# Optimization experiments

Measured on AMD Instinct MI355X. Metric: run time of the kernel, lower is better.

The kernel has to match this reference:

```python
import jax, jax.numpy as jnp
import numpy as np
from jax.ops import segment_sum

N_V = 50000   # vertices
N_E = 10000   # hyperedges
N_P = 800000  # incidence pairs
D_IN = 256
D_OUT = 256
NEG_SLOPE = 0.01


def setup_inputs() -> dict:
    key = jax.random.key(0)
    k1, k2, k3, k4, k5 = jax.random.split(key, 5)
    X = jax.random.normal(k1, (N_V, D_IN), dtype=jnp.float32)
    W = jax.random.normal(k2, (D_IN, D_OUT), dtype=jnp.float32) * (1.0 / np.sqrt(D_IN))
    b = jax.random.normal(k3, (D_OUT,), dtype=jnp.float32) * 0.01
    v_idx = jax.random.randint(k4, (N_P,), 0, N_V, dtype=jnp.int32)
    e_idx = jax.random.randint(k5, (N_P,), 0, N_E, dtype=jnp.int32)
    return {"X": X, "W": W, "b": b, "v_idx": v_idx, "e_idx": e_idx,
            "num_hyperedges": N_E}


def _mean_scatter(msg, idx, num_segments):
    # segment mean with count clamped to >=1 (empty segments -> 0)
    s = segment_sum(msg, idx, num_segments=num_segments)
    cnt = segment_sum(jnp.ones((msg.shape[0],), msg.dtype), idx,
                      num_segments=num_segments)
    return s / jnp.maximum(cnt, 1.0)[:, None]


def reference(X, W, b, v_idx, e_idx, num_hyperedges):
    # theta: linear projection  [N_V, D_OUT]
    H = X @ W + b
    # v2e mean: hyperedge features from member vertices
    e_feat = _mean_scatter(H[v_idx], e_idx, num_hyperedges)   # [N_E, D_OUT]
    # e2v mean: vertex features from incident hyperedges
    v_feat = _mean_scatter(e_feat[e_idx], v_idx, X.shape[0])  # [N_V, D_OUT]
    # leaky relu, default negative slope 0.01
    return jnp.where(v_feat >= 0, v_feat, NEG_SLOPE * v_feat)
```

## Files before the change

kernel.cpp:

```cpp
#include <hip/hip_runtime.h>

#define D 256
#define NEG_SLOPE 0.01f
#define E_PAD 192
#define V_PAD 64
#define EB 32
#define VB 64
#define NBE 313
#define NBV 782
#define CAP_E 3328
#define CAP_V 1536
#define CHUNK 8192
#define NS 8
#define DS 32

__device__ __forceinline__ unsigned short f2bf(float f) {
    union { float f; unsigned u; } x; x.f = f;
    unsigned r = x.u + 0x7fffu + ((x.u >> 16) & 1u);
    return (unsigned short)(r >> 16);
}
__device__ __forceinline__ float bf2f(unsigned short h) {
    union { float f; unsigned u; } x; x.u = ((unsigned)h) << 16;
    return x.f;
}

__global__ __launch_bounds__(256) void cvt_kernel(
        const float* __restrict__ X, unsigned short* __restrict__ Xhs, int n_v) {
    int i = blockIdx.x * blockDim.x + threadIdx.x;
    if (i >= n_v * 64) return;
    int v = i >> 6;
    int d4 = (i & 63) * 4;
    float4 val = *(const float4*)(X + (size_t)v * D + d4);
    ushort4 h;
    h.x = f2bf(val.x); h.y = f2bf(val.y); h.z = f2bf(val.z); h.w = f2bf(val.w);
    int s = d4 >> 5, wd = d4 & 31;
    *(ushort4*)(Xhs + (size_t)s * n_v * DS + (size_t)v * DS + wd) = h;
}

__global__ __launch_bounds__(256) void part_kernel(
        const int* __restrict__ v_idx, const int* __restrict__ e_idx,
        int* __restrict__ bc_e, int* __restrict__ bc_v,
        unsigned* __restrict__ pe, unsigned* __restrict__ pv, int n_p) {
    __shared__ int he[NBE], hv[NBV], beb[NBE], bvb[NBV];
    const int tid = threadIdx.x;
    const int base = blockIdx.x * CHUNK;
    for (int i = tid; i < NBE; i += 256) he[i] = 0;
    for (int i = tid; i < NBV; i += 256) hv[i] = 0;
    __syncthreads();
    #pragma unroll 4
    for (int r = 0; r < CHUNK / 256; ++r) {
        int p = base + r * 256 + tid;
        if (p < n_p) {
            atomicAdd(&he[e_idx[p] >> 5], 1);
            atomicAdd(&hv[v_idx[p] >> 6], 1);
        }
    }
    __syncthreads();
    for (int b = tid; b < NBE; b += 256) {
        int c = he[b];
        beb[b] = c ? atomicAdd(&bc_e[b], c) : 0;
        he[b] = 0;
    }
    for (int b = tid; b < NBV; b += 256) {
        int c = hv[b];
        bvb[b] = c ? atomicAdd(&bc_v[b], c) : 0;
        hv[b] = 0;
    }
    __syncthreads();
    #pragma unroll 4
    for (int r = 0; r < CHUNK / 256; ++r) {
        int p = base + r * 256 + tid;
        if (p < n_p) {
            int e = e_idx[p], v = v_idx[p];
            int b1 = e >> 5;
            int s1 = beb[b1] + atomicAdd(&he[b1], 1);
            if (s1 < CAP_E) pe[(size_t)b1 * CAP_E + s1] = (unsigned)v | ((unsigned)e << 16);
            int b2 = v >> 6;
            int s2 = bvb[b2] + atomicAdd(&hv[b2], 1);
            if (s2 < CAP_V) pv[(size_t)b2 * CAP_V + s2] = (unsigned)e | ((unsigned)v << 16);
        }
    }
}

__global__ __launch_bounds__(256) void build_e_kernel(
        const unsigned* __restrict__ pe, const int* __restrict__ bc_e,
        unsigned short* __restrict__ e_adj, int* __restrict__ e_fill, int n_e) {
    __shared__ unsigned short adj[EB * E_PAD];
    __shared__ int cnt[EB];
    const int b = blockIdx.x;
    const int tid = threadIdx.x;
    const int e0 = b * EB;
    int m = n_e - e0; if (m > EB) m = EB;
    for (int i = tid; i < EB; i += 256) cnt[i] = 0;
    __syncthreads();
    int total = bc_e[b]; if (total > CAP_E) total = CAP_E;
    for (int i = tid; i < total; i += 256) {
        unsigned p = pe[(size_t)b * CAP_E + i];
        int v = (int)(p & 0xFFFFu);
        int el = (int)(p >> 16) - e0;
        int s = atomicAdd(&cnt[el], 1);
        if (s < E_PAD) adj[el * E_PAD + s] = (unsigned short)v;
    }
    __syncthreads();
    unsigned* gout = (unsigned*)(e_adj + (size_t)e0 * E_PAD);
    const unsigned* lin = (const unsigned*)adj;
    int words = m * E_PAD / 2;
    for (int j = tid; j < words; j += 256) gout[j] = lin[j];
    for (int el = tid; el < m; el += 256) {
        int c = cnt[el]; if (c > E_PAD) c = E_PAD;
        e_fill[e0 + el] = c;
    }
}

__global__ __launch_bounds__(256) void v2e_kernel(
        const unsigned short* __restrict__ Xhs, const int* __restrict__ e_fill,
        const unsigned short* __restrict__ e_adj, float* __restrict__ Xagg,
        int n_e, int n_v) {
    const int s   = blockIdx.x;
    const int grp = threadIdx.x >> 4;
    const int sub = threadIdx.x & 15;
    const int e   = blockIdx.y * 16 + grp;
    if (e >= n_e) return;
    const unsigned short* tab = Xhs + (size_t)s * n_v * DS + (sub << 1);
    const unsigned short* adj = e_adj + (size_t)e * E_PAD;
    int cnt = e_fill[e];
    float ax = 0.f, ay = 0.f;
    int i = 0;
    for (; i + 8 <= cnt; i += 8) {
        int v0 = adj[i],   v1 = adj[i+1], v2 = adj[i+2], v3 = adj[i+3];
        int v4 = adj[i+4], v5 = adj[i+5], v6 = adj[i+6], v7 = adj[i+7];
        ushort2 a0 = *(const ushort2*)(tab + (size_t)v0 * DS);
        ushort2 a1 = *(const ushort2*)(tab + (size_t)v1 * DS);
        ushort2 a2 = *(const ushort2*)(tab + (size_t)v2 * DS);
        ushort2 a3 = *(const ushort2*)(tab + (size_t)v3 * DS);
        ushort2 a4 = *(const ushort2*)(tab + (size_t)v4 * DS);
        ushort2 a5 = *(const ushort2*)(tab + (size_t)v5 * DS);
        ushort2 a6 = *(const ushort2*)(tab + (size_t)v6 * DS);
        ushort2 a7 = *(const ushort2*)(tab + (size_t)v7 * DS);
        ax += (bf2f(a0.x) + bf2f(a1.x)) + (bf2f(a2.x) + bf2f(a3.x))
            + (bf2f(a4.x) + bf2f(a5.x)) + (bf2f(a6.x) + bf2f(a7.x));
        ay += (bf2f(a0.y) + bf2f(a1.y)) + (bf2f(a2.y) + bf2f(a3.y))
            + (bf2f(a4.y) + bf2f(a5.y)) + (bf2f(a6.y) + bf2f(a7.y));
    }
    for (; i < cnt; ++i) {
        int v = adj[i];
        ushort2 a = *(const ushort2*)(tab + (size_t)v * DS);
        ax += bf2f(a.x); ay += bf2f(a.y);
    }
    int c = cnt < 1 ? 1 : cnt;
    float inv = 1.0f / (float)c;
    float2 o; o.x = ax * inv; o.y = ay * inv;
    *(float2*)(Xagg + (size_t)e * D + s * DS + (sub << 1)) = o;
}

#define BM 64
#define BN 64
#define BK 64
#define SAK 68
#define SBN 68

__global__ __launch_bounds__(256) void gemm_kernel(
        const float* __restrict__ A, const float* __restrict__ B,
        const float* __restrict__ bias, const int* __restrict__ e_cnt,
        unsigned short* __restrict__ C, int M) {
    __shared__ float As[BM * SAK];
    __shared__ float Bs[BK * SBN];
    const int tid = threadIdx.x;
    const int tx = tid & 15, ty = tid >> 4;
    const int m0 = blockIdx.y * BM;
    const int n0 = blockIdx.x * BN;

    float acc[4][4] = {};

    for (int k0 = 0; k0 < D; k0 += BK) {
        #pragma unroll
        for (int r = 0; r < 4; ++r) {
            int l  = (tid + r * 256) * 4;
            int am = l >> 6;
            int ak = l & 63;
            int grow = m0 + am;
            float4 v = make_float4(0.f, 0.f, 0.f, 0.f);
            if (grow < M) v = *(const float4*)(A + (size_t)grow * D + k0 + ak);
            *(float4*)(&As[am * SAK + ak]) = v;
        }
        #pragma unroll
        for (int r = 0; r < 4; ++r) {
            int l  = (tid + r * 256) * 4;
            int bk = l >> 6;
            int bn = l & 63;
            float4 v = *(const float4*)(B + (size_t)(k0 + bk) * D + n0 + bn);
            *(float4*)(&Bs[bk * SBN + bn]) = v;
        }
        __syncthreads();

        #pragma unroll 8
        for (int kk = 0; kk < BK; ++kk) {
            float a0 = As[(ty * 4 + 0) * SAK + kk];
            float a1 = As[(ty * 4 + 1) * SAK + kk];
            float a2 = As[(ty * 4 + 2) * SAK + kk];
            float a3 = As[(ty * 4 + 3) * SAK + kk];
            float4 bv = *(const float4*)(Bs + kk * SBN + tx * 4);
            acc[0][0] += a0 * bv.x; acc[0][1] += a0 * bv.y; acc[0][2] += a0 * bv.z; acc[0][3] += a0 * bv.w;
            acc[1][0] += a1 * bv.x; acc[1][1] += a1 * bv.y; acc[1][2] += a1 * bv.z; acc[1][3] += a1 * bv.w;
            acc[2][0] += a2 * bv.x; acc[2][1] += a2 * bv.y; acc[2][2] += a2 * bv.z; acc[2][3] += a2 * bv.w;
            acc[3][0] += a3 * bv.x; acc[3][1] += a3 * bv.y; acc[3][2] += a3 * bv.z; acc[3][3] += a3 * bv.w;
        }
        __syncthreads();
    }

    float4 bb = *(const float4*)(bias + n0 + tx * 4);
    #pragma unroll
    for (int i = 0; i < 4; ++i) {
        int row = m0 + ty * 4 + i;
        if (row < M) {
            bool nonempty = e_cnt[row] > 0;
            ushort4 o;
            o.x = f2bf(nonempty ? acc[i][0] + bb.x : 0.f);
            o.y = f2bf(nonempty ? acc[i][1] + bb.y : 0.f);
            o.z = f2bf(nonempty ? acc[i][2] + bb.z : 0.f);
            o.w = f2bf(nonempty ? acc[i][3] + bb.w : 0.f);
            *(ushort4*)(C + (size_t)row * D + n0 + tx * 4) = o;
        }
    }
}

__global__ __launch_bounds__(256) void e2v_kernel(
        const unsigned short* __restrict__ Eh, const unsigned* __restrict__ pv,
        const int* __restrict__ bc_v, float* __restrict__ out, int n_v) {
    __shared__ unsigned short adj[VB * V_PAD];
    __shared__ int cnt[VB];
    const int b = blockIdx.x;
    const int tid = threadIdx.x;
    const int v0 = b * VB;
    for (int i = tid; i < VB; i += 256) cnt[i] = 0;
    __syncthreads();
    int total = bc_v[b]; if (total > CAP_V) total = CAP_V;
    for (int i = tid; i < total; i += 256) {
        unsigned p = pv[(size_t)b * CAP_V + i];
        int e = (int)(p & 0xFFFFu);
        int vl = (int)(p >> 16) - v0;
        int s = atomicAdd(&cnt[vl], 1);
        if (s < V_PAD) adj[vl * V_PAD + s] = (unsigned short)e;
    }
    __syncthreads();
    const int wave = tid >> 6, lane = tid & 63;
    for (int r = 0; r < VB / 4; ++r) {
        int vl = r * 4 + wave;
        int v = v0 + vl;
        if (v >= n_v) continue;
        int c = cnt[vl]; if (c > V_PAD) c = V_PAD;
        const unsigned short* a = adj + vl * V_PAD;
        float4 acc = make_float4(0.f, 0.f, 0.f, 0.f);
        int i = 0;
        for (; i + 8 <= c; i += 8) {
            int e0 = a[i],   e1 = a[i+1], e2 = a[i+2], e3 = a[i+3];
            int e4 = a[i+4], e5 = a[i+5], e6 = a[i+6], e7 = a[i+7];
            ushort4 a0 = *(const ushort4*)(Eh + (size_t)e0 * D + lane * 4);
            ushort4 a1 = *(const ushort4*)(Eh + (size_t)e1 * D + lane * 4);
            ushort4 a2 = *(const ushort4*)(Eh + (size_t)e2 * D + lane * 4);
            ushort4 a3 = *(const ushort4*)(Eh + (size_t)e3 * D + lane * 4);
            ushort4 a4 = *(const ushort4*)(Eh + (size_t)e4 * D + lane * 4);
            ushort4 a5 = *(const ushort4*)(Eh + (size_t)e5 * D + lane * 4);
            ushort4 a6 = *(const ushort4*)(Eh + (size_t)e6 * D + lane * 4);
            ushort4 a7 = *(const ushort4*)(Eh + (size_t)e7 * D + lane * 4);
            acc.x += (bf2f(a0.x) + bf2f(a1.x)) + (bf2f(a2.x) + bf2f(a3.x))
                   + (bf2f(a4.x) + bf2f(a5.x)) + (bf2f(a6.x) + bf2f(a7.x));
            acc.y += (bf2f(a0.y) + bf2f(a1.y)) + (bf2f(a2.y) + bf2f(a3.y))
                   + (bf2f(a4.y) + bf2f(a5.y)) + (bf2f(a6.y) + bf2f(a7.y));
            acc.z += (bf2f(a0.z) + bf2f(a1.z)) + (bf2f(a2.z) + bf2f(a3.z))
                   + (bf2f(a4.z) + bf2f(a5.z)) + (bf2f(a6.z) + bf2f(a7.z));
            acc.w += (bf2f(a0.w) + bf2f(a1.w)) + (bf2f(a2.w) + bf2f(a3.w))
                   + (bf2f(a4.w) + bf2f(a5.w)) + (bf2f(a6.w) + bf2f(a7.w));
        }
        for (; i < c; ++i) {
            int e = a[i];
            ushort4 x = *(const ushort4*)(Eh + (size_t)e * D + lane * 4);
            acc.x += bf2f(x.x); acc.y += bf2f(x.y); acc.z += bf2f(x.z); acc.w += bf2f(x.w);
        }
        int cc = c < 1 ? 1 : c;
        float inv = 1.0f / (float)cc;
        acc.x *= inv; acc.y *= inv; acc.z *= inv; acc.w *= inv;
        float4 o;
        o.x = acc.x >= 0.f ? acc.x : NEG_SLOPE * acc.x;
        o.y = acc.y >= 0.f ? acc.y : NEG_SLOPE * acc.y;
        o.z = acc.z >= 0.f ? acc.z : NEG_SLOPE * acc.z;
        o.w = acc.w >= 0.f ? acc.w : NEG_SLOPE * acc.w;
        *(float4*)(out + (size_t)v * D + lane * 4) = o;
    }
}

extern "C" void kernel_launch(void* const* d_in, const int* in_sizes, int n_in,
                              void* d_out, int out_size, void* d_ws, size_t ws_size,
                              hipStream_t stream) {
    const float* X    = (const float*)d_in[0];
    const float* W    = (const float*)d_in[1];
    const float* bias = (const float*)d_in[2];
    const int* v_idx  = (const int*)d_in[3];
    const int* e_idx  = (const int*)d_in[4];
    const int n_v = in_sizes[0] / D;
    const int n_p = in_sizes[3];
    const int n_e = 10000;

    char* w = (char*)d_ws;
    size_t off = 0;
    auto alloc = [&](size_t bytes) -> void* {
        void* p = w + off;
        off = (off + bytes + 255) & ~(size_t)255;
        return p;
    };
    unsigned short* Xhs = (unsigned short*)alloc((size_t)NS * n_v * DS * sizeof(unsigned short));
    float* Xagg         = (float*)alloc((size_t)n_e * D * sizeof(float));
    unsigned short* Eh  = (unsigned short*)alloc((size_t)n_e * D * sizeof(unsigned short));
    unsigned short* e_adj = (unsigned short*)alloc((size_t)n_e * E_PAD * sizeof(unsigned short));
    unsigned* pe   = (unsigned*)alloc((size_t)NBE * CAP_E * sizeof(unsigned));
    unsigned* pv   = (unsigned*)alloc((size_t)NBV * CAP_V * sizeof(unsigned));
    int*   e_fill  = (int*)alloc((size_t)n_e * sizeof(int));
    int*   bc      = (int*)alloc((size_t)(NBE + NBV) * sizeof(int));
    int*   bc_e    = bc;
    int*   bc_v    = bc + NBE;

    hipMemsetAsync(bc, 0, (size_t)(NBE + NBV) * sizeof(int), stream);

    cvt_kernel<<<(n_v * 64 + 255) / 256, 256, 0, stream>>>(X, Xhs, n_v);

    part_kernel<<<(n_p + CHUNK - 1) / CHUNK, 256, 0, stream>>>(
        v_idx, e_idx, bc_e, bc_v, pe, pv, n_p);
    build_e_kernel<<<NBE, 256, 0, stream>>>(pe, bc_e, e_adj, e_fill, n_e);

    dim3 vgrid(NS, (n_e + 15) / 16);
    v2e_kernel<<<vgrid, 256, 0, stream>>>(Xhs, e_fill, e_adj, Xagg, n_e, n_v);

    dim3 ggrid(D / BN, (n_e + BM - 1) / BM);
    gemm_kernel<<<ggrid, 256, 0, stream>>>(Xagg, W, bias, e_fill, Eh, n_e);

    e2v_kernel<<<NBV, 256, 0, stream>>>(Eh, pv, bc_v, (float*)d_out, n_v);
}
```

Measured before the change: 281.7 us.

## Slice hyperedge features by column block and split e2v into adjacency build plus sliced gather

The GEMM now writes hyperedge features in a column-sliced layout (8 slices of 32 bf16 columns), and the e2v step is split into a build_v kernel that writes a padded per-vertex adjacency list to global memory and a gather kernel whose grid runs over (slice, vertex group), mirroring v2e. Each slice of the hyperedge table is about 640KB, so the gathers for one slice can stay in cache. Output is written with nontemporal stores. The cost is an extra kernel launch and a round trip of v_adj (about 6.4MB) through global memory, and each gather now moves only 4 bytes per lane.

```diff
diff --git a/kernel.cpp b/kernel.cpp
--- a/kernel.cpp
+++ b/kernel.cpp
@@ -23,6 +23,9 @@
     union { float f; unsigned u; } x; x.u = ((unsigned)h) << 16;
     return x.f;
 }
+__device__ __forceinline__ float lrelu(float x) {
+    return x >= 0.f ? x : NEG_SLOPE * x;
+}
 
 __global__ __launch_bounds__(256) void cvt_kernel(
         const float* __restrict__ X, unsigned short* __restrict__ Xhs, int n_v) {
@@ -109,6 +112,36 @@
     for (int el = tid; el < m; el += 256) {
         int c = cnt[el]; if (c > E_PAD) c = E_PAD;
         e_fill[e0 + el] = c;
+    }
+}
+
+__global__ __launch_bounds__(256) void build_v_kernel(
+        const unsigned* __restrict__ pv, const int* __restrict__ bc_v,
+        unsigned short* __restrict__ v_adj, int* __restrict__ v_fill, int n_v) {
+    __shared__ unsigned short adj[VB * V_PAD];
+    __shared__ int cnt[VB];
+    const int b = blockIdx.x;
+    const int tid = threadIdx.x;
+    const int v0 = b * VB;
+    int m = n_v - v0; if (m > VB) m = VB;
+    for (int i = tid; i < VB; i += 256) cnt[i] = 0;
+    __syncthreads();
+    int total = bc_v[b]; if (total > CAP_V) total = CAP_V;
+    for (int i = tid; i < total; i += 256) {
+        unsigned p = pv[(size_t)b * CAP_V + i];
+        int e = (int)(p & 0xFFFFu);
+        int vl = (int)(p >> 16) - v0;
+        int s = atomicAdd(&cnt[vl], 1);
+        if (s < V_PAD) adj[vl * V_PAD + s] = (unsigned short)e;
+    }
+    __syncthreads();
+    unsigned* gout = (unsigned*)(v_adj + (size_t)v0 * V_PAD);
+    const unsigned* lin = (const unsigned*)adj;
+    int words = m * V_PAD / 2;
+    for (int j = tid; j < words; j += 256) gout[j] = lin[j];
+    for (int vl = tid; vl < m; vl += 256) {
+        int c = cnt[vl]; if (c > V_PAD) c = V_PAD;
+        v_fill[v0 + vl] = c;
     }
 }
 
@@ -162,7 +195,7 @@
 __global__ __launch_bounds__(256) void gemm_kernel(
         const float* __restrict__ A, const float* __restrict__ B,
         const float* __restrict__ bias, const int* __restrict__ e_cnt,
-        unsigned short* __restrict__ C, int M) {
+        unsigned short* __restrict__ Ehs, int M) {
     __shared__ float As[BM * SAK];
     __shared__ float Bs[BK * SBN];
     const int tid = threadIdx.x;
@@ -208,7 +241,10 @@
         __syncthreads();
     }
 
-    float4 bb = *(const float4*)(bias + n0 + tx * 4);
+    const int col = n0 + tx * 4;
+    const int sl  = col >> 5;
+    const int wd  = col & 31;
+    float4 bb = *(const float4*)(bias + col);
     #pragma unroll
     for (int i = 0; i < 4; ++i) {
         int row = m0 + ty * 4 + i;
@@ -219,74 +255,53 @@
             o.y = f2bf(nonempty ? acc[i][1] + bb.y : 0.f);
             o.z = f2bf(nonempty ? acc[i][2] + bb.z : 0.f);
             o.w = f2bf(nonempty ? acc[i][3] + bb.w : 0.f);
-            *(ushort4*)(C + (size_t)row * D + n0 + tx * 4) = o;
+            *(ushort4*)(Ehs + (size_t)sl * M * DS + (size_t)row * DS + wd) = o;
         }
     }
 }
 
 __global__ __launch_bounds__(256) void e2v_kernel(
-        const unsigned short* __restrict__ Eh, const unsigned* __restrict__ pv,
-        const int* __restrict__ bc_v, float* __restrict__ out, int n_v) {
-    __shared__ unsigned short adj[VB * V_PAD];
-    __shared__ int cnt[VB];
-    const int b = blockIdx.x;
-    const int tid = threadIdx.x;
-    const int v0 = b * VB;
-    for (int i = tid; i < VB; i += 256) cnt[i] = 0;
-    __syncthreads();
-    int total = bc_v[b]; if (total > CAP_V) total = CAP_V;
-    for (int i = tid; i < total; i += 256) {
-        unsigned p = pv[(size_t)b * CAP_V + i];
-        int e = (int)(p & 0xFFFFu);
-        int vl = (int)(p >> 16) - v0;
-        int s = atomicAdd(&cnt[vl], 1);
-        if (s < V_PAD) adj[vl * V_PAD + s] = (unsigned short)e;
-    }
-    __syncthreads();
-    const int wave = tid >> 6, lane = tid & 63;
-    for (int r = 0; r < VB / 4; ++r) {
-        int vl = r * 4 + wave;
-        int v = v0 + vl;
-        if (v >= n_v) continue;
-        int c = cnt[vl]; if (c > V_PAD) c = V_PAD;
-        const unsigned short* a = adj + vl * V_PAD;
-        float4 acc = make_float4(0.f, 0.f, 0.f, 0.f);
-        int i = 0;
-        for (; i + 8 <= c; i += 8) {
-            int e0 = a[i],   e1 = a[i+1], e2 = a[i+2], e3 = a[i+3];
-            int e4 = a[i+4], e5 = a[i+5], e6 = a[i+6], e7 = a[i+7];
-            ushort4 a0 = *(const ushort4*)(Eh + (size_t)e0 * D + lane * 4);
-            ushort4 a1 = *(const ushort4*)(Eh + (size_t)e1 * D + lane * 4);
-            ushort4 a2 = *(const ushort4*)(Eh + (size_t)e2 * D + lane * 4);
-            ushort4 a3 = *(const ushort4*)(Eh + (size_t)e3 * D + lane * 4);
-            ushort4 a4 = *(const ushort4*)(Eh + (size_t)e4 * D + lane * 4);
-            ushort4 a5 = *(const ushort4*)(Eh + (size_t)e5 * D + lane * 4);
-            ushort4 a6 = *(const ushort4*)(Eh + (size_t)e6 * D + lane * 4);
-            ushort4 a7 = *(const ushort4*)(Eh + (size_t)e7 * D + lane * 4);
-            acc.x += (bf2f(a0.x) + bf2f(a1.x)) + (bf2f(a2.x) + bf2f(a3.x))
-                   + (bf2f(a4.x) + bf2f(a5.x)) + (bf2f(a6.x) + bf2f(a7.x));
-            acc.y += (bf2f(a0.y) + bf2f(a1.y)) + (bf2f(a2.y) + bf2f(a3.y))
-                   + (bf2f(a4.y) + bf2f(a5.y)) + (bf2f(a6.y) + bf2f(a7.y));
-            acc.z += (bf2f(a0.z) + bf2f(a1.z)) + (bf2f(a2.z) + bf2f(a3.z))
-                   + (bf2f(a4.z) + bf2f(a5.z)) + (bf2f(a6.z) + bf2f(a7.z));
-            acc.w += (bf2f(a0.w) + bf2f(a1.w)) + (bf2f(a2.w) + bf2f(a3.w))
-                   + (bf2f(a4.w) + bf2f(a5.w)) + (bf2f(a6.w) + bf2f(a7.w));
-        }
-        for (; i < c; ++i) {
-            int e = a[i];
-            ushort4 x = *(const ushort4*)(Eh + (size_t)e * D + lane * 4);
-            acc.x += bf2f(x.x); acc.y += bf2f(x.y); acc.z += bf2f(x.z); acc.w += bf2f(x.w);
-        }
-        int cc = c < 1 ? 1 : c;
-        float inv = 1.0f / (float)cc;
-        acc.x *= inv; acc.y *= inv; acc.z *= inv; acc.w *= inv;
-        float4 o;
-        o.x = acc.x >= 0.f ? acc.x : NEG_SLOPE * acc.x;
-        o.y = acc.y >= 0.f ? acc.y : NEG_SLOPE * acc.y;
-        o.z = acc.z >= 0.f ? acc.z : NEG_SLOPE * acc.z;
-        o.w = acc.w >= 0.f ? acc.w : NEG_SLOPE * acc.w;
-        *(float4*)(out + (size_t)v * D + lane * 4) = o;
-    }
+        const unsigned short* __restrict__ Ehs, const int* __restrict__ v_fill,
+        const unsigned short* __restrict__ v_adj, float* __restrict__ out,
+        int n_v, int n_e) {
+    const int s   = blockIdx.x;
+    const int grp = threadIdx.x >> 4;
+    const int sub = threadIdx.x & 15;
+    const int v   = blockIdx.y * 16 + grp;
+    if (v >= n_v) return;
+    const unsigned short* tab = Ehs + (size_t)s * n_e * DS + (sub << 1);
+    const unsigned short* adj = v_adj + (size_t)v * V_PAD;
+    int cnt = v_fill[v];
+    float ax = 0.f, ay = 0.f;
+    int i = 0;
+    for (; i + 8 <= cnt; i += 8) {
+        int e0 = adj[i],   e1 = adj[i+1], e2 = adj[i+2], e3 = adj[i+3];
+        int e4 = adj[i+4], e5 = adj[i+5], e6 = adj[i+6], e7 = adj[i+7];
+        ushort2 a0 = *(const ushort2*)(tab + (size_t)e0 * DS);
+        ushort2 a1 = *(const ushort2*)(tab + (size_t)e1 * DS);
+        ushort2 a2 = *(const ushort2*)(tab + (size_t)e2 * DS);
+        ushort2 a3 = *(const ushort2*)(tab + (size_t)e3 * DS);
+        ushort2 a4 = *(const ushort2*)(tab + (size_t)e4 * DS);
+        ushort2 a5 = *(const ushort2*)(tab + (size_t)e5 * DS);
+        ushort2 a6 = *(const ushort2*)(tab + (size_t)e6 * DS);
+        ushort2 a7 = *(const ushort2*)(tab + (size_t)e7 * DS);
+        ax += (bf2f(a0.x) + bf2f(a1.x)) + (bf2f(a2.x) + bf2f(a3.x))
+            + (bf2f(a4.x) + bf2f(a5.x)) + (bf2f(a6.x) + bf2f(a7.x));
+        ay += (bf2f(a0.y) + bf2f(a1.y)) + (bf2f(a2.y) + bf2f(a3.y))
+            + (bf2f(a4.y) + bf2f(a5.y)) + (bf2f(a6.y) + bf2f(a7.y));
+    }
+    for (; i < cnt; ++i) {
+        int e = adj[i];
+        ushort2 a = *(const ushort2*)(tab + (size_t)e * DS);
+        ax += bf2f(a.x); ay += bf2f(a.y);
+    }
+    int c = cnt < 1 ? 1 : cnt;
+    float inv = 1.0f / (float)c;
+    float2 o;
+    o.x = lrelu(ax * inv);
+    o.y = lrelu(ay * inv);
+    __builtin_nontemporal_store(o.x, out + (size_t)v * D + s * DS + (sub << 1));
+    __builtin_nontemporal_store(o.y, out + (size_t)v * D + s * DS + (sub << 1) + 1);
 }
 
 extern "C" void kernel_launch(void* const* d_in, const int* in_sizes, int n_in,
@@ -310,11 +325,13 @@
     };
     unsigned short* Xhs = (unsigned short*)alloc((size_t)NS * n_v * DS * sizeof(unsigned short));
     float* Xagg         = (float*)alloc((size_t)n_e * D * sizeof(float));
-    unsigned short* Eh  = (unsigned short*)alloc((size_t)n_e * D * sizeof(unsigned short));
+    unsigned short* Ehs = (unsigned short*)alloc((size_t)NS * n_e * DS * sizeof(unsigned short));
     unsigned short* e_adj = (unsigned short*)alloc((size_t)n_e * E_PAD * sizeof(unsigned short));
+    unsigned short* v_adj = (unsigned short*)alloc((size_t)n_v * V_PAD * sizeof(unsigned short));
     unsigned* pe   = (unsigned*)alloc((size_t)NBE * CAP_E * sizeof(unsigned));
     unsigned* pv   = (unsigned*)alloc((size_t)NBV * CAP_V * sizeof(unsigned));
     int*   e_fill  = (int*)alloc((size_t)n_e * sizeof(int));
+    int*   v_fill  = (int*)alloc((size_t)n_v * sizeof(int));
     int*   bc      = (int*)alloc((size_t)(NBE + NBV) * sizeof(int));
     int*   bc_e    = bc;
     int*   bc_v    = bc + NBE;
@@ -326,12 +343,14 @@
     part_kernel<<<(n_p + CHUNK - 1) / CHUNK, 256, 0, stream>>>(
         v_idx, e_idx, bc_e, bc_v, pe, pv, n_p);
     build_e_kernel<<<NBE, 256, 0, stream>>>(pe, bc_e, e_adj, e_fill, n_e);
+    build_v_kernel<<<NBV, 256, 0, stream>>>(pv, bc_v, v_adj, v_fill, n_v);
 
     dim3 vgrid(NS, (n_e + 15) / 16);
     v2e_kernel<<<vgrid, 256, 0, stream>>>(Xhs, e_fill, e_adj, Xagg, n_e, n_v);
 
     dim3 ggrid(D / BN, (n_e + BM - 1) / BM);
-    gemm_kernel<<<ggrid, 256, 0, stream>>>(Xagg, W, bias, e_fill, Eh, n_e);
-
-    e2v_kernel<<<NBV, 256, 0, stream>>>(Eh, pv, bc_v, (float*)d_out, n_v);
-}
+    gemm_kernel<<<ggrid, 256, 0, stream>>>(Xagg, W, bias, e_fill, Ehs, n_e);
+
+    dim3 egrid(NS, (n_v + 15) / 16);
+    e2v_kernel<<<egrid, 256, 0, stream>>>(Ehs, v_fill, v_adj, (float*)d_out, n_v, n_e);
+}
```

Measured after the change: 291.4 us. 1.03x slower.
